# Performance work log

Measured on AMD Instinct MI355X. Metric: run time of the kernel, lower is better.

The kernel has to match this reference:

```python
import jax, jax.numpy as jnp
import numpy as np

N_HEADS = 16


def apply_rotary_emb(x, cos, sin):
    # x: [B, H, S, hd]; cos/sin: [S, hd//2] (broadcast over B, H)
    xr = x.reshape(x.shape[:-1] + (-1, 2))
    r, i = xr[..., 0], xr[..., 1]
    a = r * cos - i * sin
    b = i * cos + r * sin
    return jnp.stack([a, b], axis=-1).reshape(x.shape).astype(x.dtype)


def setup_inputs() -> dict:
    key = jax.random.key(0)
    ks = jax.random.split(key, 7)
    B, S, D = 2, 2048, 1024
    hd = D // N_HEADS
    x = jax.random.normal(ks[0], (B, S, D), dtype=jnp.float32)
    freqs_cos = jax.random.uniform(ks[1], (S, hd // 2), dtype=jnp.float32)
    freqs_sin = jax.random.uniform(ks[2], (S, hd // 2), dtype=jnp.float32)
    sc = 1.0 / np.sqrt(D)
    Wq = jax.random.normal(ks[3], (D, D), dtype=jnp.float32) * sc
    Wk = jax.random.normal(ks[4], (D, D), dtype=jnp.float32) * sc
    Wv = jax.random.normal(ks[5], (D, D), dtype=jnp.float32) * sc
    Wo = jax.random.normal(ks[6], (D, D), dtype=jnp.float32) * sc
    return {"x": x, "freqs_cos": freqs_cos, "freqs_sin": freqs_sin,
            "Wq": Wq, "Wk": Wk, "Wv": Wv, "Wo": Wo}


def reference(x, freqs_cos, freqs_sin, Wq, Wk, Wv, Wo):
    B, S, D = x.shape
    H = N_HEADS
    hd = D // H
    # QKV projections (nn.Linear: x @ W.T)
    q = (x @ Wq.T).reshape(B, S, H, hd).transpose(0, 2, 1, 3)
    k = (x @ Wk.T).reshape(B, S, H, hd).transpose(0, 2, 1, 3)
    v = (x @ Wv.T).reshape(B, S, H, hd).transpose(0, 2, 1, 3)
    q = apply_rotary_emb(q, freqs_cos, freqs_sin)
    k = apply_rotary_emb(k, freqs_cos, freqs_sin)
    # causal SDPA (scale = 1/sqrt(head_dim), as in F.scaled_dot_product_attention)
    scores = jnp.einsum("bhqd,bhkd->bhqk", q, k) * (1.0 / np.sqrt(hd))
    causal = jnp.tril(jnp.ones((S, S), dtype=bool))
    scores = jnp.where(causal, scores, -jnp.inf)
    probs = jax.nn.softmax(scores, axis=-1)
    attn_out = jnp.einsum("bhqk,bhkd->bhqd", probs, v)
    attn_cat = attn_out.transpose(0, 2, 1, 3).reshape(B, S, D)
    return attn_cat @ Wo.T
```

## Files before the change

kernel.cpp:

```cpp
#include <hip/hip_runtime.h>
#include <hip/hip_bf16.h>
#include <cstdint>

typedef __attribute__((ext_vector_type(8))) short short8;
typedef __attribute__((ext_vector_type(4))) float f32x4;

#define B_  2
#define S_  2048
#define D_  1024
#define H_  16
#define HD  64

static __device__ __forceinline__ float bf2f(unsigned int u16) {
    union { unsigned int i; float f; } v; v.i = u16 << 16; return v.f;
}
static __device__ __forceinline__ unsigned short f2bf(float f) {
    union { float f; unsigned int i; } v; v.f = f;
    unsigned int r = v.i + 0x7FFFu + ((v.i >> 16) & 1u);
    return (unsigned short)(r >> 16);
}
static __device__ __forceinline__ unsigned pack_bf16(float hi, float lo) {
    union { float f; unsigned u; } h, l;
    h.f = hi; l.f = lo;
    return __builtin_amdgcn_perm(h.u + 0x8000u, l.u + 0x8000u, 0x07060302);
}
static __device__ __forceinline__ void load_lds_16B(const unsigned short* g, unsigned short* l) {
    __builtin_amdgcn_global_load_lds(
        (const __attribute__((address_space(1))) unsigned int*)g,
        (__attribute__((address_space(3))) unsigned int*)l, 16, 0, 0);
}

__global__ void cvt_f32_bf16(const float* __restrict__ src,
                             unsigned short* __restrict__ dst, int n4) {
    int i = blockIdx.x * 256 + threadIdx.x;
    if (i >= n4) return;
    float4 f = ((const float4*)src)[i];
    uint2 o;
    o.x = (unsigned int)f2bf(f.x) | ((unsigned int)f2bf(f.y) << 16);
    o.y = (unsigned int)f2bf(f.z) | ((unsigned int)f2bf(f.w) << 16);
    ((uint2*)dst)[i] = o;
}

__global__ void cvt_w4(const float* __restrict__ w0, const float* __restrict__ w1,
                       const float* __restrict__ w2, const float* __restrict__ w3,
                       unsigned short* __restrict__ dst) {
    int bid = blockIdx.x;
    int wsel = bid >> 10;
    const float* s = wsel == 0 ? w0 : wsel == 1 ? w1 : wsel == 2 ? w2 : w3;
    int i = (bid & 1023) * 256 + threadIdx.x;
    float4 f = ((const float4*)s)[i];
    uint2 o;
    o.x = (unsigned int)f2bf(f.x) | ((unsigned int)f2bf(f.y) << 16);
    o.y = (unsigned int)f2bf(f.z) | ((unsigned int)f2bf(f.w) << 16);
    ((uint2*)dst)[(size_t)wsel * 262144 + i] = o;
}

__global__ __launch_bounds__(256) void qkv_gemm(
    const unsigned short* __restrict__ xbf,
    const unsigned short* __restrict__ wq,
    const unsigned short* __restrict__ wk,
    const unsigned short* __restrict__ wv,
    unsigned short* __restrict__ qb,
    unsigned short* __restrict__ kb,
    unsigned short* __restrict__ vb)
{
    __shared__ unsigned short As[128 * 32];
    __shared__ unsigned short Bs[128 * 32];

    const int tid  = threadIdx.x;
    const int w    = tid >> 6, lane = tid & 63;
    const int l15  = lane & 15, quad = lane >> 4;
    const int wrow = (w >> 1) * 64, wcol = (w & 1) * 64;

    const int m0 = blockIdx.x * 128;
    const int nc = blockIdx.y * 128;
    const int sel = nc >> 10;
    const int n0 = nc & 1023;
    const unsigned short* __restrict__ W = sel == 0 ? wq : (sel == 1 ? wk : wv);
    unsigned short* __restrict__ Out = sel == 0 ? qb : (sel == 1 ? kb : vb);

    const int lr = lane >> 2, lc = (lane & 3) * 8;
    const unsigned short* ga = xbf + (size_t)(m0 + w * 16 + lr) * 1024 + lc;
    const unsigned short* gb = W   + (size_t)(n0 + w * 16 + lr) * 1024 + lc;
    unsigned short* la0 = As + (w * 16) * 32;
    unsigned short* la1 = As + (64 + w * 16) * 32;
    unsigned short* lb0 = Bs + (w * 16) * 32;
    unsigned short* lb1 = Bs + (64 + w * 16) * 32;

    f32x4 acc[4][4] = {};

    for (int k0 = 0; k0 < 1024; k0 += 32) {
        __syncthreads();
        load_lds_16B(ga + k0,             la0);
        load_lds_16B(ga + 64 * 1024 + k0, la1);
        load_lds_16B(gb + k0,             lb0);
        load_lds_16B(gb + 64 * 1024 + k0, lb1);
        __syncthreads();

        short8 a[4], b[4];
#pragma unroll
        for (int i = 0; i < 4; i++)
            a[i] = *(const short8*)&As[(wrow + i * 16 + l15) * 32 + quad * 8];
#pragma unroll
        for (int j = 0; j < 4; j++)
            b[j] = *(const short8*)&Bs[(wcol + j * 16 + l15) * 32 + quad * 8];
#pragma unroll
        for (int i = 0; i < 4; i++)
#pragma unroll
            for (int j = 0; j < 4; j++)
                acc[i][j] = __builtin_amdgcn_mfma_f32_16x16x32_bf16(a[i], b[j], acc[i][j], 0, 0, 0);
    }

#pragma unroll
    for (int i = 0; i < 4; i++) {
#pragma unroll
        for (int r = 0; r < 4; r++) {
            int m = m0 + wrow + i * 16 + quad * 4 + r;
            int bb = m >> 11, s = m & 2047;
#pragma unroll
            for (int j = 0; j < 4; j++) {
                int n = n0 + wcol + j * 16 + l15;
                int h = n >> 6, d = n & 63;
                Out[(((size_t)(bb * H_ + h) * S_) + s) * HD + d] = f2bf(acc[i][j][r]);
            }
        }
    }
}

__global__ __launch_bounds__(256) void out_gemm(
    const unsigned short* __restrict__ A,
    const unsigned short* __restrict__ Bt,
    float* __restrict__ C)
{
    __shared__ unsigned short As[128 * 32];
    __shared__ unsigned short Bs[128 * 32];

    const int tid  = threadIdx.x;
    const int w    = tid >> 6, lane = tid & 63;
    const int l15  = lane & 15, quad = lane >> 4;
    const int wrow = (w >> 1) * 64, wcol = (w & 1) * 64;

    const int m0 = blockIdx.x * 128;
    const int n0 = blockIdx.y * 128;

    const int lr = lane >> 2, lc = (lane & 3) * 8;
    const unsigned short* ga = A  + (size_t)(m0 + w * 16 + lr) * 1024 + lc;
    const unsigned short* gb = Bt + (size_t)(n0 + w * 16 + lr) * 1024 + lc;
    unsigned short* la0 = As + (w * 16) * 32;
    unsigned short* la1 = As + (64 + w * 16) * 32;
    unsigned short* lb0 = Bs + (w * 16) * 32;
    unsigned short* lb1 = Bs + (64 + w * 16) * 32;

    f32x4 acc[4][4] = {};

    for (int k0 = 0; k0 < 1024; k0 += 32) {
        __syncthreads();
        load_lds_16B(ga + k0,             la0);
        load_lds_16B(ga + 64 * 1024 + k0, la1);
        load_lds_16B(gb + k0,             lb0);
        load_lds_16B(gb + 64 * 1024 + k0, lb1);
        __syncthreads();

        short8 a[4], b[4];
#pragma unroll
        for (int i = 0; i < 4; i++)
            a[i] = *(const short8*)&As[(wrow + i * 16 + l15) * 32 + quad * 8];
#pragma unroll
        for (int j = 0; j < 4; j++)
            b[j] = *(const short8*)&Bs[(wcol + j * 16 + l15) * 32 + quad * 8];
#pragma unroll
        for (int i = 0; i < 4; i++)
#pragma unroll
            for (int j = 0; j < 4; j++)
                acc[i][j] = __builtin_amdgcn_mfma_f32_16x16x32_bf16(a[i], b[j], acc[i][j], 0, 0, 0);
    }

#pragma unroll
    for (int i = 0; i < 4; i++)
#pragma unroll
        for (int r = 0; r < 4; r++) {
            int m = m0 + wrow + i * 16 + quad * 4 + r;
#pragma unroll
            for (int j = 0; j < 4; j++)
                C[(size_t)m * 1024 + n0 + wcol + j * 16 + l15] = acc[i][j][r];
        }
}

__global__ void rope_qk(unsigned short* __restrict__ qb,
                        unsigned short* __restrict__ kb,
                        const float* __restrict__ fcos,
                        const float* __restrict__ fsin)
{
    int idx = blockIdx.x * 256 + threadIdx.x;
    int t  = idx & 31;
    int s  = (idx >> 5) & (S_ - 1);
    int bh = idx >> 16;
    float c  = fcos[s * 32 + t];
    float si = fsin[s * 32 + t];
    size_t off = ((size_t)bh * S_ + s) * HD + 2 * t;

    unsigned int* qp = (unsigned int*)(qb + off);
    unsigned int u = *qp;
    float r = bf2f(u & 0xffffu), im = bf2f(u >> 16);
    *qp = pack_bf16(im * c + r * si, r * c - im * si);

    unsigned int* kp = (unsigned int*)(kb + off);
    u = *kp;
    r = bf2f(u & 0xffffu); im = bf2f(u >> 16);
    *kp = pack_bf16(im * c + r * si, r * c - im * si);
}

__global__ __launch_bounds__(256) void v_transpose(
    const unsigned short* __restrict__ vb,
    unsigned short* __restrict__ vT)
{
    __shared__ unsigned short T[64][72];
    const int bh = blockIdx.x;
    const int j0 = blockIdx.y * 64;
    const int tid = threadIdx.x;
    const int vdg = tid >> 5, vp = tid & 31;
    const unsigned short* vptr = vb + ((size_t)bh * S_ + j0 + 2 * vp) * HD + vdg * 8;
    uint4 v0 = *(const uint4*)vptr;
    uint4 v1 = *(const uint4*)(vptr + HD);
    const unsigned* a0 = (const unsigned*)&v0;
    const unsigned* a1 = (const unsigned*)&v1;
#pragma unroll
    for (int c = 0; c < 4; c++) {
        *(unsigned*)&T[vdg * 8 + 2 * c][2 * vp]     = __builtin_amdgcn_perm(a1[c], a0[c], 0x05040100);
        *(unsigned*)&T[vdg * 8 + 2 * c + 1][2 * vp] = __builtin_amdgcn_perm(a1[c], a0[c], 0x07060302);
    }
    __syncthreads();
    const int d = tid >> 3, js = (tid & 7) * 8;
#pragma unroll
    for (int dd = 0; dd < 2; dd++) {
        short8 row = *(const short8*)&T[dd * 32 + d][js];
        *(short8*)(vT + ((size_t)bh * HD + dd * 32 + d) * S_ + j0 + js) = row;
    }
}

__global__ __launch_bounds__(256) void flash_attn_mfma(
    const unsigned short* __restrict__ qb,
    const unsigned short* __restrict__ kb,
    const unsigned short* __restrict__ vT,
    unsigned short* __restrict__ attnc)
{
    __shared__ __attribute__((aligned(1024))) unsigned short Ks[2][64][32];
    __shared__ __attribute__((aligned(1024))) unsigned short Vt[64][64];
    __shared__ unsigned short Pls[4][16][72];

    const int bh   = blockIdx.x;
    const int qtb  = blockIdx.y;
    const int jj = qtb & 7, mm = qtb >> 3;
    const int qt = (mm == 0) ? jj : (mm == 1) ? 31 - jj : (mm == 2) ? 8 + jj : 23 - jj;

    const int b    = bh >> 4, h = bh & 15;
    const int tid  = threadIdx.x;
    const int w    = tid >> 6;
    const int lane = tid & 63;
    const int l15  = lane & 15;
    const int quad = lane >> 4;

    const size_t bhS = (size_t)bh * S_;
    const unsigned short* __restrict__ vTb = vT + (size_t)bh * HD * S_;

    short8 qfrag[2];
    {
        const unsigned short* qp = qb + (bhS + qt * 64 + w * 16 + l15) * HD + quad * 8;
        qfrag[0] = *(const short8*)(qp);
        qfrag[1] = *(const short8*)(qp + 32);
    }

    const int ksrow  = lane >> 2;
    const int ksslot = (lane & 3) ^ ((lane >> 3) & 3);
    const int vsrow  = lane >> 3;
    const int vsslot = (lane & 7) ^ vsrow;

    const int ckq = (quad ^ ((l15 >> 1) & 3)) << 4;
    const int s7  = l15 & 7;

    f32x4 O[4] = {};
    float mrow = -INFINITY;
    float lrow = 0.0f;
    const float sc = 0.125f * 1.44269504f;

    for (int jt = 0; jt <= qt; jt++) {
        const int j0 = jt * 64;
        {
            const unsigned short* kg = kb + (bhS + j0 + w * 16 + ksrow) * HD + ksslot * 8;
            load_lds_16B(kg,      &Ks[0][w * 16][0]);
            load_lds_16B(kg + 32, &Ks[1][w * 16][0]);
        }
        {
            const unsigned short* vg = vTb + (size_t)(w * 16 + vsrow) * S_ + j0 + vsslot * 8;
            load_lds_16B(vg,          &Vt[w * 16][0]);
            load_lds_16B(vg + 8 * S_, &Vt[w * 16 + 8][0]);
        }
        __syncthreads();

        const bool diag  = (jt == qt);
        const int  nsub  = diag ? (w + 1) : 4;
        const int  kgmax = (nsub + 1) >> 1;

        f32x4 Sacc[4];
        float tmax = -INFINITY;
        for (int sub = 0; sub < nsub; sub++) {
            f32x4 s = {};
#pragma unroll
            for (int kh = 0; kh < 2; kh++) {
                int bo = ((sub * 16 + l15) << 6) + ckq;
                short8 kf = *(const short8*)((const char*)&Ks[kh][0][0] + bo);
                s = __builtin_amdgcn_mfma_f32_16x16x32_bf16(kf, qfrag[kh], s, 0, 0, 0);
            }
#pragma unroll
            for (int r = 0; r < 4; r++) {
                float v = s[r] * sc;
                if (diag && (sub * 16 + quad * 4 + r > w * 16 + l15)) v = -INFINITY;
                s[r] = v;
                tmax = fmaxf(tmax, v);
            }
            Sacc[sub] = s;
        }
        tmax = fmaxf(tmax, __shfl_xor(tmax, 16, 64));
        tmax = fmaxf(tmax, __shfl_xor(tmax, 32, 64));

        if (__any(tmax > mrow + 8.0f)) {
            float mnew = fmaxf(mrow, tmax);
            float ccr  = __builtin_amdgcn_exp2f(mrow - mnew);
            lrow *= ccr;
#pragma unroll
            for (int r = 0; r < 4; r++) {
                float ccq = __shfl(ccr, quad * 4 + r, 64);
#pragma unroll
                for (int dt = 0; dt < 4; dt++) O[dt][r] *= ccq;
            }
            mrow = mnew;
        }

        float psum = 0.0f;
        for (int sub = 0; sub < nsub; sub++) {
            f32x4 s = Sacc[sub];
            float p0 = __builtin_amdgcn_exp2f(s[0] - mrow);
            float p1 = __builtin_amdgcn_exp2f(s[1] - mrow);
            float p2 = __builtin_amdgcn_exp2f(s[2] - mrow);
            float p3 = __builtin_amdgcn_exp2f(s[3] - mrow);
            psum += (p0 + p1) + (p2 + p3);
            uint2 pk;
            pk.x = pack_bf16(p1, p0);
            pk.y = pack_bf16(p3, p2);
            *(uint2*)&Pls[w][l15][sub * 16 + quad * 4] = pk;
        }
        if (diag) {
            for (int sub = nsub; sub < 2 * kgmax; sub++) {
                uint2 z; z.x = 0u; z.y = 0u;
                *(uint2*)&Pls[w][l15][sub * 16 + quad * 4] = z;
            }
        }
        psum += __shfl_xor(psum, 16, 64);
        psum += __shfl_xor(psum, 32, 64);
        lrow += psum;

        for (int kg = 0; kg < kgmax; kg++) {
            short8 pf = *(const short8*)&Pls[w][l15][kg * 32 + quad * 8];
#pragma unroll
            for (int dt = 0; dt < 4; dt++) {
                int row = dt * 16 + l15;
                int slot = (((kg << 2) | quad) ^ s7) << 4;
                short8 vf = *(const short8*)((const char*)&Vt[0][0] + (row << 7) + slot);
                O[dt] = __builtin_amdgcn_mfma_f32_16x16x32_bf16(pf, vf, O[dt], 0, 0, 0);
            }
        }
        __syncthreads();
    }

    float inv = 1.0f / lrow;
#pragma unroll
    for (int r = 0; r < 4; r++) {
        float invq = __shfl(inv, quad * 4 + r, 64);
        int qabs = qt * 64 + w * 16 + quad * 4 + r;
        unsigned short* op = attnc + (((size_t)b * S_ + qabs) * H_ + h) * HD + l15;
#pragma unroll
        for (int dt = 0; dt < 4; dt++)
            op[dt * 16] = f2bf(O[dt][r] * invq);
    }
}

extern "C" void kernel_launch(void* const* d_in, const int* in_sizes, int n_in,
                              void* d_out, int out_size, void* d_ws, size_t ws_size,
                              hipStream_t stream) {
    const float* x    = (const float*)d_in[0];
    const float* fcos = (const float*)d_in[1];
    const float* fsin = (const float*)d_in[2];
    const float* Wq   = (const float*)d_in[3];
    const float* Wk   = (const float*)d_in[4];
    const float* Wv   = (const float*)d_in[5];
    const float* Wo   = (const float*)d_in[6];
    float* out = (float*)d_out;

    unsigned short* ws = (unsigned short*)d_ws;
    unsigned short* xbf = ws;
    unsigned short* wqb = xbf + 4096 * 1024;
    unsigned short* wkb = wqb + 1024 * 1024;
    unsigned short* wvb = wkb + 1024 * 1024;
    unsigned short* wob = wvb + 1024 * 1024;
    unsigned short* qb  = wob + 1024 * 1024;
    unsigned short* kb  = qb + 4096 * 1024;
    unsigned short* vb  = kb + 4096 * 1024;
    unsigned short* attnc = vb + 4096 * 1024;
    unsigned short* vT = xbf;

    cvt_f32_bf16<<<4096, 256, 0, stream>>>(x, xbf, 4096 * 1024 / 4);
    cvt_w4<<<4096, 256, 0, stream>>>(Wq, Wk, Wv, Wo, wqb);

    qkv_gemm<<<dim3(32, 24), 256, 0, stream>>>(xbf, wqb, wkb, wvb, qb, kb, vb);

    v_transpose<<<dim3(32, 32), 256, 0, stream>>>(vb, vT);

    rope_qk<<<8192, 256, 0, stream>>>(qb, kb, fcos, fsin);

    flash_attn_mfma<<<dim3(32, 32), 256, 0, stream>>>(qb, kb, vT, attnc);

    out_gemm<<<dim3(32, 8), 256, 0, stream>>>(attnc, wob, out);
}
```

Measured before the change: 215.9 us.

## Double-buffer K/V tiles in flash attention and fold softmax scale into RoPE

Flash attention now double-buffers the K and V^T LDS tiles, issuing async loads for the next key tile before computing the current one. It waits with explicit vmcnt counts and raw s_barrier instead of __syncthreads. The softmax scale (1/sqrt(hd)·log2e) is folded into Q during the RoPE pass, removing a multiply per score, and s_setprio brackets the MFMA sections. LDS usage grows to hold two buffers, and Q is rounded to bf16 after scaling, which slightly changes numerics.

```diff
diff --git a/kernel.cpp b/kernel.cpp
--- a/kernel.cpp
+++ b/kernel.cpp
@@ -191,18 +191,20 @@
                         const float* __restrict__ fcos,
                         const float* __restrict__ fsin)
 {
+    const float SCQ = 0.125f * 1.44269504f;
     int idx = blockIdx.x * 256 + threadIdx.x;
     int t  = idx & 31;
     int s  = (idx >> 5) & (S_ - 1);
     int bh = idx >> 16;
     float c  = fcos[s * 32 + t];
     float si = fsin[s * 32 + t];
+    float cq = c * SCQ, sq = si * SCQ;
     size_t off = ((size_t)bh * S_ + s) * HD + 2 * t;
 
     unsigned int* qp = (unsigned int*)(qb + off);
     unsigned int u = *qp;
     float r = bf2f(u & 0xffffu), im = bf2f(u >> 16);
-    *qp = pack_bf16(im * c + r * si, r * c - im * si);
+    *qp = pack_bf16(im * cq + r * sq, r * cq - im * sq);
 
     unsigned int* kp = (unsigned int*)(kb + off);
     u = *kp;
@@ -244,8 +246,8 @@
     const unsigned short* __restrict__ vT,
     unsigned short* __restrict__ attnc)
 {
-    __shared__ __attribute__((aligned(1024))) unsigned short Ks[2][64][32];
-    __shared__ __attribute__((aligned(1024))) unsigned short Vt[64][64];
+    __shared__ __attribute__((aligned(1024))) unsigned short Ks[2][2][64][32];
+    __shared__ __attribute__((aligned(1024))) unsigned short Vt[2][64][64];
     __shared__ unsigned short Pls[4][16][72];
 
     const int bh   = blockIdx.x;
@@ -281,21 +283,28 @@
     f32x4 O[4] = {};
     float mrow = -INFINITY;
     float lrow = 0.0f;
-    const float sc = 0.125f * 1.44269504f;
+
+    auto STAGE = [&](int jt, int bufi) {
+        const int j0 = jt * 64;
+        const unsigned short* kg = kb + (bhS + j0 + w * 16 + ksrow) * HD + ksslot * 8;
+        load_lds_16B(kg,      &Ks[bufi][0][w * 16][0]);
+        load_lds_16B(kg + 32, &Ks[bufi][1][w * 16][0]);
+        const unsigned short* vg = vTb + (size_t)(w * 16 + vsrow) * S_ + j0 + vsslot * 8;
+        load_lds_16B(vg,          &Vt[bufi][w * 16][0]);
+        load_lds_16B(vg + 8 * S_, &Vt[bufi][w * 16 + 8][0]);
+    };
+
+    STAGE(0, 0);
 
     for (int jt = 0; jt <= qt; jt++) {
-        const int j0 = jt * 64;
-        {
-            const unsigned short* kg = kb + (bhS + j0 + w * 16 + ksrow) * HD + ksslot * 8;
-            load_lds_16B(kg,      &Ks[0][w * 16][0]);
-            load_lds_16B(kg + 32, &Ks[1][w * 16][0]);
-        }
-        {
-            const unsigned short* vg = vTb + (size_t)(w * 16 + vsrow) * S_ + j0 + vsslot * 8;
-            load_lds_16B(vg,          &Vt[w * 16][0]);
-            load_lds_16B(vg + 8 * S_, &Vt[w * 16 + 8][0]);
-        }
-        __syncthreads();
+        const int cur = jt & 1;
+        if (jt < qt) {
+            STAGE(jt + 1, cur ^ 1);
+            asm volatile("s_waitcnt vmcnt(4)" ::: "memory");
+        } else {
+            asm volatile("s_waitcnt vmcnt(0)" ::: "memory");
+        }
+        __builtin_amdgcn_s_barrier();
 
         const bool diag  = (jt == qt);
         const int  nsub  = diag ? (w + 1) : 4;
@@ -305,15 +314,17 @@
         float tmax = -INFINITY;
         for (int sub = 0; sub < nsub; sub++) {
             f32x4 s = {};
+            __builtin_amdgcn_s_setprio(1);
 #pragma unroll
             for (int kh = 0; kh < 2; kh++) {
                 int bo = ((sub * 16 + l15) << 6) + ckq;
-                short8 kf = *(const short8*)((const char*)&Ks[kh][0][0] + bo);
+                short8 kf = *(const short8*)((const char*)&Ks[cur][kh][0][0] + bo);
                 s = __builtin_amdgcn_mfma_f32_16x16x32_bf16(kf, qfrag[kh], s, 0, 0, 0);
             }
+            __builtin_amdgcn_s_setprio(0);
 #pragma unroll
             for (int r = 0; r < 4; r++) {
-                float v = s[r] * sc;
+                float v = s[r];
                 if (diag && (sub * 16 + quad * 4 + r > w * 16 + l15)) v = -INFINITY;
                 s[r] = v;
                 tmax = fmaxf(tmax, v);
@@ -359,17 +370,21 @@
         psum += __shfl_xor(psum, 32, 64);
         lrow += psum;
 
+        __builtin_amdgcn_s_setprio(1);
         for (int kg = 0; kg < kgmax; kg++) {
             short8 pf = *(const short8*)&Pls[w][l15][kg * 32 + quad * 8];
 #pragma unroll
             for (int dt = 0; dt < 4; dt++) {
                 int row = dt * 16 + l15;
                 int slot = (((kg << 2) | quad) ^ s7) << 4;
-                short8 vf = *(const short8*)((const char*)&Vt[0][0] + (row << 7) + slot);
+                short8 vf = *(const short8*)((const char*)&Vt[cur][0][0] + (row << 7) + slot);
                 O[dt] = __builtin_amdgcn_mfma_f32_16x16x32_bf16(pf, vf, O[dt], 0, 0, 0);
             }
         }
-        __syncthreads();
+        __builtin_amdgcn_s_setprio(0);
+
+        asm volatile("" ::: "memory");
+        __builtin_amdgcn_s_barrier();
     }
 
     float inv = 1.0f / lrow;
```

Result: slower. 221.5 us (+2.6%).
